# Performance work log

Measured on AMD Instinct MI355X. Metric: run time of the kernel, lower is better.

Reference implementation:

```python
import jax, jax.numpy as jnp
import numpy as np

D_MODEL = 1024
NUM_HEADS = 16
D_HEAD = D_MODEL // NUM_HEADS
LN_EPS = 1e-5


def setup_inputs() -> dict:
    key = jax.random.key(0)
    ks = jax.random.split(key, 10)
    s = 1.0 / np.sqrt(D_MODEL)
    inp = {
        "batch": jax.random.normal(ks[0], (4, 2048, D_MODEL), dtype=jnp.float32),
        "wq": jax.random.uniform(ks[1], (D_MODEL, D_MODEL), jnp.float32, -s, s),
        "bq": jax.random.uniform(ks[2], (D_MODEL,), jnp.float32, -s, s),
        "wk": jax.random.uniform(ks[3], (D_MODEL, D_MODEL), jnp.float32, -s, s),
        "bk": jax.random.uniform(ks[4], (D_MODEL,), jnp.float32, -s, s),
        "wv": jax.random.uniform(ks[5], (D_MODEL, D_MODEL), jnp.float32, -s, s),
        "bv": jax.random.uniform(ks[6], (D_MODEL,), jnp.float32, -s, s),
        "wo": jax.random.uniform(ks[7], (D_MODEL, D_MODEL), jnp.float32, -s, s),
        "bo": jax.random.uniform(ks[8], (D_MODEL,), jnp.float32, -s, s),
        "ln_g": jnp.ones((D_MODEL,), jnp.float32),
        "ln_b": jnp.zeros((D_MODEL,), jnp.float32),
    }
    return inp


def reference(batch, wq, bq, wk, bk, wv, bv, wo, bo, ln_g, ln_b):
    B, S, D = batch.shape
    # QKV projections (torch Linear: x @ W.T + b)
    q = (batch @ wq.T + bq).reshape(B, S, NUM_HEADS, D_HEAD)
    k = (batch @ wk.T + bk).reshape(B, S, NUM_HEADS, D_HEAD)
    v = (batch @ wv.T + bv).reshape(B, S, NUM_HEADS, D_HEAD)
    # attention scores [B, H, S, S]
    scores = jnp.einsum("bqhd,bkhd->bhqk", q, k) / np.sqrt(D_HEAD).astype(np.float32)
    # (original masked_fill is not in-place -> mask has no effect; omitted)
    probs = jax.nn.softmax(scores, axis=-1)
    attn = jnp.einsum("bhqk,bkhd->bqhd", probs, v).reshape(B, S, D)
    residual = attn @ wo.T + bo  # dropout = identity (eval mode)
    x = batch + residual
    mu = jnp.mean(x, axis=-1, keepdims=True)
    var = jnp.mean(jnp.square(x - mu), axis=-1, keepdims=True)
    return (x - mu) / jnp.sqrt(var + LN_EPS) * ln_g + ln_b
```

## Files before the change

kernel.cpp:

```cpp
#include <hip/hip_runtime.h>

typedef __bf16 bf16_t;
typedef __bf16 v8bf __attribute__((ext_vector_type(8)));
typedef __bf16 v4bf __attribute__((ext_vector_type(4)));
typedef float  v4f  __attribute__((ext_vector_type(4)));

#define D_MODEL 1024
#define NHEAD   16
#define DHEAD   64
#define SEQ     2048
#define BATCH   4
#define ROWS    (BATCH*SEQ)

#define GLD16(g, l) __builtin_amdgcn_global_load_lds( \
    (const __attribute__((address_space(1))) void*)(g), \
    (__attribute__((address_space(3))) void*)(l), 16, 0, 0)

#define BAR asm volatile("s_barrier" ::: "memory")

__global__ __launch_bounds__(256) void k_prep(const float* __restrict__ batch,
                                              const float* __restrict__ wq,
                                              const float* __restrict__ wk,
                                              const float* __restrict__ wv,
                                              const float* __restrict__ wo,
                                              const float* __restrict__ bq,
                                              const float* __restrict__ bk,
                                              const float* __restrict__ bv,
                                              bf16_t* __restrict__ Xb,
                                              bf16_t* __restrict__ Wqkv,
                                              bf16_t* __restrict__ Wob,
                                              float* __restrict__ bqkv) {
    int t = threadIdx.x;
    for (int bid = blockIdx.x; bid < 12300; bid += 2048) {
        const float* src; bf16_t* dst; int idx;
        if (bid < 8192)       { src = batch; dst = Xb;             idx = bid * 256 + t; }
        else if (bid < 9216)  { src = wq;    dst = Wqkv;           idx = (bid - 8192) * 256 + t; }
        else if (bid < 10240) { src = wk;    dst = Wqkv + 1048576; idx = (bid - 9216) * 256 + t; }
        else if (bid < 11264) { src = wv;    dst = Wqkv + 2097152; idx = (bid - 10240) * 256 + t; }
        else if (bid < 12288) { src = wo;    dst = Wob;            idx = (bid - 11264) * 256 + t; }
        else {
            int i = (bid - 12288) * 256 + t;
            if (i < 1024) bqkv[i] = bq[i];
            else if (i < 2048) bqkv[i] = bk[i - 1024];
            else if (i < 3072) bqkv[i] = bv[i - 2048];
            continue;
        }
        float4 f = ((const float4*)src)[idx];
        v4bf o;
        o[0] = (bf16_t)f.x; o[1] = (bf16_t)f.y; o[2] = (bf16_t)f.z; o[3] = (bf16_t)f.w;
        ((v4bf*)dst)[idx] = o;
    }
}

__global__ __launch_bounds__(512, 2) void k_gemm256(
    const bf16_t* __restrict__ A, const bf16_t* __restrict__ Bm,
    const float* __restrict__ bias, bf16_t* __restrict__ C, float qmul)
{
    __shared__ bf16_t As[2][2][256 * 32];
    __shared__ bf16_t Bs[2][2][256 * 32];

    const int K = 1024;
    int bid = blockIdx.x;
    int wg = (bid & 7) * 48 + (bid >> 3);
    int m_idx = wg / 12, n_idx = wg % 12;
    int m0 = m_idx << 8, n0 = n_idx << 8;

    int t = threadIdx.x;
    int lane = t & 63, quad = lane >> 4, ln = lane & 15;
    int w = t >> 6, wr = w >> 2, wc = w & 3;

    int cl = (t & 3) ^ ((t >> 3) & 3);
    const bf16_t* Ag = A  + (size_t)(m0 + (t >> 2)) * K + cl * 8;
    const bf16_t* Bg = Bm + (size_t)(n0 + (t >> 2)) * K + cl * 8;
    int wb = w << 9;

#define STA(bufv, khv, kc) { const bf16_t* g_ = Ag + (kc) + ((khv) << 5); \
    GLD16(g_, &As[bufv][khv][wb]); GLD16(g_ + 131072, &As[bufv][khv][wb + 4096]); }
#define STB(bufv, khv, kc) { const bf16_t* g_ = Bg + (kc) + ((khv) << 5); \
    GLD16(g_, &Bs[bufv][khv][wb]); GLD16(g_ + 131072, &Bs[bufv][khv][wb + 4096]); }

    int rsw = (quad ^ ((ln >> 1) & 3)) << 3;
    int aofs = (wr * 128 + ln) * 32 + rsw;
    int bofs = (wc * 64 + ln) * 32 + rsw;

#define LDA(dst, bufv, mhv) { \
    dst[0] = *(const v8bf*)&AB_[aofs + (mhv) * 2048]; \
    dst[1] = *(const v8bf*)&AB_[aofs + (mhv) * 2048 + 512]; \
    dst[2] = *(const v8bf*)&AB_[aofs + (mhv) * 2048 + 1024]; \
    dst[3] = *(const v8bf*)&AB_[aofs + (mhv) * 2048 + 1536]; }
#define LDAF(dst, bufv, khv, mhv) { const bf16_t* AB_ = &As[bufv][khv][0]; LDA(dst, bufv, mhv) }
#define LDBF(dst, bufv, khv) { const bf16_t* BB_ = &Bs[bufv][khv][0]; \
    dst[0] = *(const v8bf*)&BB_[bofs]; \
    dst[1] = *(const v8bf*)&BB_[bofs + 512]; \
    dst[2] = *(const v8bf*)&BB_[bofs + 1024]; \
    dst[3] = *(const v8bf*)&BB_[bofs + 1536]; }

    v4f acc[8][4];
#pragma unroll
    for (int i = 0; i < 8; i++)
#pragma unroll
        for (int j = 0; j < 4; j++) acc[i][j] = (v4f){0.f, 0.f, 0.f, 0.f};

    v8bf aX[4], aY[4], bX[4], bY[4];

#define MF(AC, BC, M0) \
    __builtin_amdgcn_s_setprio(1); \
    acc[(M0)+0][0] = __builtin_amdgcn_mfma_f32_16x16x32_bf16(AC[0], BC[0], acc[(M0)+0][0], 0, 0, 0); \
    acc[(M0)+0][1] = __builtin_amdgcn_mfma_f32_16x16x32_bf16(AC[0], BC[1], acc[(M0)+0][1], 0, 0, 0); \
    acc[(M0)+0][2] = __builtin_amdgcn_mfma_f32_16x16x32_bf16(AC[0], BC[2], acc[(M0)+0][2], 0, 0, 0); \
    acc[(M0)+0][3] = __builtin_amdgcn_mfma_f32_16x16x32_bf16(AC[0], BC[3], acc[(M0)+0][3], 0, 0, 0); \
    acc[(M0)+1][0] = __builtin_amdgcn_mfma_f32_16x16x32_bf16(AC[1], BC[0], acc[(M0)+1][0], 0, 0, 0); \
    acc[(M0)+1][1] = __builtin_amdgcn_mfma_f32_16x16x32_bf16(AC[1], BC[1], acc[(M0)+1][1], 0, 0, 0); \
    acc[(M0)+1][2] = __builtin_amdgcn_mfma_f32_16x16x32_bf16(AC[1], BC[2], acc[(M0)+1][2], 0, 0, 0); \
    acc[(M0)+1][3] = __builtin_amdgcn_mfma_f32_16x16x32_bf16(AC[1], BC[3], acc[(M0)+1][3], 0, 0, 0); \
    acc[(M0)+2][0] = __builtin_amdgcn_mfma_f32_16x16x32_bf16(AC[2], BC[0], acc[(M0)+2][0], 0, 0, 0); \
    acc[(M0)+2][1] = __builtin_amdgcn_mfma_f32_16x16x32_bf16(AC[2], BC[1], acc[(M0)+2][1], 0, 0, 0); \
    acc[(M0)+2][2] = __builtin_amdgcn_mfma_f32_16x16x32_bf16(AC[2], BC[2], acc[(M0)+2][2], 0, 0, 0); \
    acc[(M0)+2][3] = __builtin_amdgcn_mfma_f32_16x16x32_bf16(AC[2], BC[3], acc[(M0)+2][3], 0, 0, 0); \
    acc[(M0)+3][0] = __builtin_amdgcn_mfma_f32_16x16x32_bf16(AC[3], BC[0], acc[(M0)+3][0], 0, 0, 0); \
    acc[(M0)+3][1] = __builtin_amdgcn_mfma_f32_16x16x32_bf16(AC[3], BC[1], acc[(M0)+3][1], 0, 0, 0); \
    acc[(M0)+3][2] = __builtin_amdgcn_mfma_f32_16x16x32_bf16(AC[3], BC[2], acc[(M0)+3][2], 0, 0, 0); \
    acc[(M0)+3][3] = __builtin_amdgcn_mfma_f32_16x16x32_bf16(AC[3], BC[3], acc[(M0)+3][3], 0, 0, 0); \
    __builtin_amdgcn_s_setprio(0);

#define TAIL_W6 { asm volatile("s_waitcnt vmcnt(6)" ::: "memory"); BAR; __builtin_amdgcn_sched_barrier(0); }
#define TAIL_W4 { asm volatile("s_waitcnt vmcnt(4)" ::: "memory"); BAR; __builtin_amdgcn_sched_barrier(0); }
#define TAIL_W0 { asm volatile("s_waitcnt vmcnt(0)" ::: "memory"); BAR; __builtin_amdgcn_sched_barrier(0); }
#define TAIL_B  { BAR; __builtin_amdgcn_sched_barrier(0); }

    STA(0, 0, 0); STB(0, 0, 0);
    STA(0, 1, 0); STB(0, 1, 0);
    STA(1, 0, 64); STB(1, 0, 64);
    asm volatile("s_waitcnt vmcnt(8)" ::: "memory");
    BAR; __builtin_amdgcn_sched_barrier(0);
    LDAF(aX, 0, 0, 0); LDBF(bX, 0, 0);

#define TILE(b, kc, S1, S2, S3, S4, T1, T3, P4B, P4LD) \
    S1; LDAF(aY, b, 0, 1);                    MF(aX, bX, 0); T1; \
    S2; LDBF(bY, b, 1); LDAF(aX, b, 1, 0);    MF(aY, bX, 4); TAIL_B; \
    S3; LDAF(aY, b, 1, 1);                    MF(aX, bY, 0); T3; \
    S4; if (P4LD) { LDBF(bX, P4B, 0); LDAF(aX, P4B, 0, 0); } \
                                              MF(aY, bY, 4); TAIL_B;

    int kb = 0;
#pragma unroll 1
    for (int tp = 0; tp < 7; ++tp, kb += 128) {
        TILE(0, kb, STA(1, 1, kb + 64), STB(1, 1, kb + 64),
                    STA(0, 0, kb + 128), STB(0, 0, kb + 128),
                    TAIL_W6, TAIL_W6, 1, 1)
        TILE(1, kb + 64, STA(0, 1, kb + 128), STB(0, 1, kb + 128),
                         STA(1, 0, kb + 192), STB(1, 0, kb + 192),
                         TAIL_W6, TAIL_W6, 0, 1)
    }
    TILE(0, 896, STA(1, 1, 960), STB(1, 1, 960), , ,
                 TAIL_W6, TAIL_W4, 1, 1)
    { const int b = 1;
      LDAF(aY, b, 0, 1);                    MF(aX, bX, 0); TAIL_W0;
      LDBF(bY, b, 1); LDAF(aX, b, 1, 0);    MF(aY, bX, 4); TAIL_B;
      LDAF(aY, b, 1, 1);                    MF(aX, bY, 0); TAIL_B;
                                            MF(aY, bY, 4);
    }

#undef TILE
#undef MF
#undef TAIL_W6
#undef TAIL_W4
#undef TAIL_W0
#undef TAIL_B
#undef LDA
#undef LDAF
#undef LDBF
#undef STA
#undef STB

#pragma unroll
    for (int m = 0; m < 8; m++) {
#pragma unroll
        for (int r = 0; r < 4; r++) {
            int row = m0 + wr * 128 + m * 16 + quad * 4 + r;
#pragma unroll
            for (int n = 0; n < 4; n++) {
                int col = n0 + wc * 64 + n * 16 + ln;
                float v = acc[m][n][r] + bias[col];
                if (col < 1024) v *= qmul;
                C[(size_t)row * 3072 + col] = (bf16_t)v;
            }
        }
    }
}

__global__ __launch_bounds__(256, 3) void k_gemm_bt(
    const bf16_t* __restrict__ A, const bf16_t* __restrict__ Bm,
    const float* __restrict__ bias, const float* __restrict__ resid,
    bf16_t* __restrict__ Cb, float* __restrict__ Cf,
    int M, int N, int K, int qcols, float qmul)
{
    __shared__ bf16_t As[3][128 * 32];
    __shared__ bf16_t Bs[3][128 * 32];

    int nTile = N >> 7;
    int x = blockIdx.x & 7, g = blockIdx.x >> 3;
    int n_idx = g % nTile;
    int m_idx = (g / nTile) * 8 + x;
    int m0 = m_idx << 7;
    int n0 = n_idx << 7;
    int t = threadIdx.x;
    int w = t >> 6, lane = t & 63, quad = lane >> 4, ln = lane & 15;
    int wm = (w >> 1) << 6, wn = (w & 1) << 6;

    int srow = lane >> 2;
    int scol = ((lane & 3) ^ ((lane >> 3) & 3)) << 3;
    const bf16_t* Ag0 = A  + (size_t)(m0 + w * 16 +      srow) * K + scol;
    const bf16_t* Ag1 = A  + (size_t)(m0 + w * 16 + 64 + srow) * K + scol;
    const bf16_t* Bg0 = Bm + (size_t)(n0 + w * 16 +      srow) * K + scol;
    const bf16_t* Bg1 = Bm + (size_t)(n0 + w * 16 + 64 + srow) * K + scol;
    int lo0 = (w * 16) * 32, lo1 = (w * 16 + 64) * 32;

    v4f acc[4][4];
#pragma unroll
    for (int i = 0; i < 4; i++)
#pragma unroll
        for (int j = 0; j < 4; j++) acc[i][j] = (v4f){0.f, 0.f, 0.f, 0.f};

    bf16_t* aPrev = As[2]; bf16_t* aCur = As[0]; bf16_t* aNext = As[1];
    bf16_t* bPrev = Bs[2]; bf16_t* bCur = Bs[0]; bf16_t* bNext = Bs[1];

    GLD16(Ag0, aCur + lo0);
    GLD16(Ag1, aCur + lo1);
    GLD16(Bg0, bCur + lo0);
    GLD16(Bg1, bCur + lo1);
    GLD16(Ag0 + 32, aNext + lo0);
    GLD16(Ag1 + 32, aNext + lo1);
    GLD16(Bg0 + 32, bNext + lo0);
    GLD16(Bg1 + 32, bNext + lo1);

    int sw = (ln >> 1) & 3;
    for (int k0 = 0; k0 < K; k0 += 32) {
        if (k0 + 32 < K) asm volatile("s_waitcnt vmcnt(4)" ::: "memory");
        else             asm volatile("s_waitcnt vmcnt(0)" ::: "memory");
        __builtin_amdgcn_s_barrier();
        __builtin_amdgcn_sched_barrier(0);
        if (k0 + 64 < K) {
            GLD16(Ag0 + k0 + 64, aPrev + lo0);
            GLD16(Ag1 + k0 + 64, aPrev + lo1);
            GLD16(Bg0 + k0 + 64, bPrev + lo0);
            GLD16(Bg1 + k0 + 64, bPrev + lo1);
        }
        v8bf af[4], bfr[4];
#pragma unroll
        for (int mt = 0; mt < 4; mt++)
            af[mt] = *(const v8bf*)&aCur[(wm + mt * 16 + ln) * 32 + ((quad ^ sw) << 3)];
#pragma unroll
        for (int nt = 0; nt < 4; nt++)
            bfr[nt] = *(const v8bf*)&bCur[(wn + nt * 16 + ln) * 32 + ((quad ^ sw) << 3)];
#pragma unroll
        for (int mt = 0; mt < 4; mt++)
#pragma unroll
            for (int nt = 0; nt < 4; nt++)
                acc[mt][nt] = __builtin_amdgcn_mfma_f32_16x16x32_bf16(af[mt], bfr[nt], acc[mt][nt], 0, 0, 0);
        bf16_t* ta = aPrev; aPrev = aCur; aCur = aNext; aNext = ta;
        bf16_t* tb = bPrev; bPrev = bCur; bCur = bNext; bNext = tb;
    }

#pragma unroll
    for (int mt = 0; mt < 4; mt++) {
#pragma unroll
        for (int r = 0; r < 4; r++) {
            int row = m0 + wm + mt * 16 + quad * 4 + r;
#pragma unroll
            for (int nt = 0; nt < 4; nt++) {
                int col = n0 + wn + nt * 16 + ln;
                float v = acc[mt][nt][r] + bias[col];
                if (Cf) Cf[(size_t)row * N + col] = v + resid[(size_t)row * N + col];
                else {
                    if (col < qcols) v *= qmul;
                    Cb[(size_t)row * N + col] = (bf16_t)v;
                }
            }
        }
    }
}

__global__ __launch_bounds__(256) void k_transpose_v(const bf16_t* __restrict__ qkv,
                                                     bf16_t* __restrict__ vt) {
    __shared__ bf16_t tile[64 * 72];
    int bid = blockIdx.x;
    int st = bid & 31, bh = bid >> 5, b = bh >> 4, h = bh & 15;
    int t = threadIdx.x;
    const bf16_t* src = qkv + (size_t)(b * SEQ + st * 64) * 3072 + 2048 + h * 64;
#pragma unroll
    for (int i = 0; i < 2; i++) {
        int c = t + i * 256, row = c >> 3, c8 = (c & 7) << 3;
        *(uint4*)&tile[row * 72 + c8] = *(const uint4*)(src + (size_t)row * 3072 + c8);
    }
    __syncthreads();
    bf16_t* dst = vt + (size_t)bh * DHEAD * SEQ + st * 64;
#pragma unroll
    for (int i = 0; i < 2; i++) {
        int c = t + i * 256, d = c >> 3, s8 = (c & 7) << 3;
        v8bf o;
#pragma unroll
        for (int j = 0; j < 8; j++) o[j] = tile[(s8 + j) * 72 + d];
        *(v8bf*)(dst + (size_t)d * SEQ + s8) = o;
    }
}

__global__ __launch_bounds__(256, 4) void k_attn(const bf16_t* __restrict__ qkv,
                                                 const bf16_t* __restrict__ vt,
                                                 bf16_t* __restrict__ attn) {
    __shared__ bf16_t Ks[2][64 * 64];
    __shared__ bf16_t Vs[2][64 * 64];

    int bid = blockIdx.x;
    int xcd = bid & 7, g = bid >> 3;
    int qt = g & 15;
    int bh = ((g >> 4) << 3) | xcd;
    int b = bh >> 4, h = bh & 15;
    int t = threadIdx.x, w = t >> 6, lane = t & 63, quad = lane >> 4, ln = lane & 15;
    int q0 = qt * 128 + w * 32;

    v8bf qf[2][2];
#pragma unroll
    for (int qs = 0; qs < 2; qs++) {
        const bf16_t* Qp = qkv + (size_t)(b * SEQ + q0 + qs * 16 + ln) * 3072 + h * 64 + quad * 8;
        qf[qs][0] = *(const v8bf*)Qp;
        qf[qs][1] = *(const v8bf*)(Qp + 32);
    }

    int srow = lane >> 3;
    int scolK = ((lane & 7) ^ ((lane >> 3) & 3) ^ ((w & 1) << 2)) << 3;
    int scolV = ((lane & 7) ^ (lane >> 3)) << 3;
    const bf16_t* Kg0 = qkv + (size_t)(b * SEQ + w * 8 +      srow) * 3072 + 1024 + h * 64 + scolK;
    const bf16_t* Kg1 = qkv + (size_t)(b * SEQ + w * 8 + 32 + srow) * 3072 + 1024 + h * 64 + scolK;
    const bf16_t* Vg0 = vt + (size_t)bh * DHEAD * SEQ + (size_t)(w * 8 +      srow) * SEQ + scolV;
    const bf16_t* Vg1 = vt + (size_t)bh * DHEAD * SEQ + (size_t)(w * 8 + 32 + srow) * SEQ + scolV;
    int ko0 = (w * 8) * 64, ko1 = (w * 8 + 32) * 64;

    int gk = (ln & 3) | (((ln >> 2) & 1) << 2);
    int gv = ln & 7;
    int rrbase = ((ln >> 2) << 3) + (ln & 3);
    int o0 = (rrbase) * 64,       o1 = (rrbase + 4) * 64;
    int o2 = (rrbase + 32) * 64,  o3 = (rrbase + 36) * 64;

    const v4f z4 = (v4f){0.f, 0.f, 0.f, 0.f};
    v8bf ones8;
#pragma unroll
    for (int j = 0; j < 8; j++) ones8[j] = (bf16_t)1.0f;

    v4f o[2][4];
#pragma unroll
    for (int qs = 0; qs < 2; qs++)
#pragma unroll
        for (int d = 0; d < 4; d++) o[qs][d] = z4;
    v4f den[2] = {z4, z4};

    GLD16(Kg0, &Ks[0][ko0]);
    GLD16(Kg1, &Ks[0][ko1]);
    GLD16(Vg0, &Vs[0][ko0]);
    GLD16(Vg1, &Vs[0][ko1]);

    int buf = 0;
    for (int kt = 0; kt < SEQ; kt += 64, buf ^= 1) {
        __syncthreads();
        if (kt + 64 < SEQ) {
            GLD16(Kg0 + (size_t)(kt + 64) * 3072, &Ks[buf ^ 1][ko0]);
            GLD16(Kg1 + (size_t)(kt + 64) * 3072, &Ks[buf ^ 1][ko1]);
            GLD16(Vg0 + kt + 64, &Vs[buf ^ 1][ko0]);
            GLD16(Vg1 + kt + 64, &Vs[buf ^ 1][ko1]);
        }

        const bf16_t* Kb = &Ks[buf][0];
        v4f s0[4], s1[4];
        int rof[4] = {o0, o1, o2, o3};
#pragma unroll
        for (int nt = 0; nt < 4; nt++) {
            v8bf kf0 = *(const v8bf*)&Kb[rof[nt] + ((quad ^ gk) << 3)];
            v8bf kf1 = *(const v8bf*)&Kb[rof[nt] + (((quad | 4) ^ gk) << 3)];
            s0[nt] = __builtin_amdgcn_mfma_f32_16x16x32_bf16(kf0, qf[0][0], z4, 0, 0, 0);
            s0[nt] = __builtin_amdgcn_mfma_f32_16x16x32_bf16(kf1, qf[0][1], s0[nt], 0, 0, 0);
            s1[nt] = __builtin_amdgcn_mfma_f32_16x16x32_bf16(kf0, qf[1][0], z4, 0, 0, 0);
            s1[nt] = __builtin_amdgcn_mfma_f32_16x16x32_bf16(kf1, qf[1][1], s1[nt], 0, 0, 0);
        }

#pragma unroll
        for (int tk = 0; tk < 2; tk++) {
            v8bf vfd[4];
#pragma unroll
            for (int d = 0; d < 4; d++)
                vfd[d] = *(const v8bf*)&Vs[buf][(d * 16 + ln) * 64 + (((tk * 4 + quad) ^ gv) << 3)];
#pragma unroll
            for (int qs = 0; qs < 2; qs++) {
                v4f* s = qs ? s1 : s0;
                float e0 = __builtin_amdgcn_exp2f(s[2 * tk][0]);
                float e1 = __builtin_amdgcn_exp2f(s[2 * tk][1]);
                float e2 = __builtin_amdgcn_exp2f(s[2 * tk][2]);
                float e3 = __builtin_amdgcn_exp2f(s[2 * tk][3]);
                float e4 = __builtin_amdgcn_exp2f(s[2 * tk + 1][0]);
                float e5 = __builtin_amdgcn_exp2f(s[2 * tk + 1][1]);
                float e6 = __builtin_amdgcn_exp2f(s[2 * tk + 1][2]);
                float e7 = __builtin_amdgcn_exp2f(s[2 * tk + 1][3]);
                v8bf pf;
                pf[0] = (bf16_t)e0; pf[1] = (bf16_t)e1; pf[2] = (bf16_t)e2; pf[3] = (bf16_t)e3;
                pf[4] = (bf16_t)e4; pf[5] = (bf16_t)e5; pf[6] = (bf16_t)e6; pf[7] = (bf16_t)e7;
                den[qs] = __builtin_amdgcn_mfma_f32_16x16x32_bf16(pf, ones8, den[qs], 0, 0, 0);
#pragma unroll
                for (int d = 0; d < 4; d++)
                    o[qs][d] = __builtin_amdgcn_mfma_f32_16x16x32_bf16(pf, vfd[d], o[qs][d], 0, 0, 0);
            }
        }
    }

#pragma unroll
    for (int qs = 0; qs < 2; qs++) {
        int rowg = b * SEQ + q0 + qs * 16;
#pragma unroll
        for (int r = 0; r < 4; r++) {
            float inv = 1.f / den[qs][r];
#pragma unroll
            for (int d = 0; d < 4; d++)
                attn[(size_t)(rowg + quad * 4 + r) * D_MODEL + h * 64 + d * 16 + ln] =
                    (bf16_t)(o[qs][d][r] * inv);
        }
    }
}

__global__ __launch_bounds__(256) void k_layernorm(const float* __restrict__ y,
                                                   const float* __restrict__ g,
                                                   const float* __restrict__ beta,
                                                   float* __restrict__ out) {
    __shared__ float rs[4], rq[4];
    int row = blockIdx.x, t = threadIdx.x;
    int w = t >> 6, lane = t & 63;
    float4 v = ((const float4*)(y + (size_t)row * D_MODEL))[t];
    float s = v.x + v.y + v.z + v.w;
    float q = v.x * v.x + v.y * v.y + v.z * v.z + v.w * v.w;
#pragma unroll
    for (int off = 1; off < 64; off <<= 1) {
        s += __shfl_xor(s, off);
        q += __shfl_xor(q, off);
    }
    if (lane == 0) { rs[w] = s; rq[w] = q; }
    __syncthreads();
    s = rs[0] + rs[1] + rs[2] + rs[3];
    q = rq[0] + rq[1] + rq[2] + rq[3];
    float mu = s * (1.f / D_MODEL);
    float var = q * (1.f / D_MODEL) - mu * mu;
    float rstd = rsqrtf(var + 1e-5f);
    float4 gg = ((const float4*)g)[t];
    float4 bb = ((const float4*)beta)[t];
    float4 o;
    o.x = (v.x - mu) * rstd * gg.x + bb.x;
    o.y = (v.y - mu) * rstd * gg.y + bb.y;
    o.z = (v.z - mu) * rstd * gg.z + bb.z;
    o.w = (v.w - mu) * rstd * gg.w + bb.w;
    ((float4*)(out + (size_t)row * D_MODEL))[t] = o;
}

extern "C" void kernel_launch(void* const* d_in, const int* in_sizes, int n_in,
                              void* d_out, int out_size, void* d_ws, size_t ws_size,
                              hipStream_t stream) {
    const float* batch = (const float*)d_in[0];
    const float* wq = (const float*)d_in[1];
    const float* bq = (const float*)d_in[2];
    const float* wk = (const float*)d_in[3];
    const float* bk = (const float*)d_in[4];
    const float* wv = (const float*)d_in[5];
    const float* bv = (const float*)d_in[6];
    const float* wo = (const float*)d_in[7];
    const float* bo = (const float*)d_in[8];
    const float* ln_g = (const float*)d_in[9];
    const float* ln_b = (const float*)d_in[10];
    float* out = (float*)d_out;

    char* ws = (char*)d_ws;
    size_t offXb   = 0;
    size_t offWqkv = offXb + (size_t)ROWS * D_MODEL * 2;
    size_t offWo   = offWqkv + (size_t)3072 * 1024 * 2;
    size_t offBias = offWo + (size_t)1024 * 1024 * 2;
    size_t offQKV  = offBias + 3072 * 4;
    size_t offAttn = offQKV + (size_t)ROWS * 3072 * 2;
    size_t total   = offAttn + (size_t)ROWS * D_MODEL * 2;
    if (ws_size < total) return;

    bf16_t* Xb   = (bf16_t*)(ws + offXb);
    bf16_t* Vt   = (bf16_t*)(ws + offXb);
    bf16_t* Wqkv = (bf16_t*)(ws + offWqkv);
    bf16_t* Wob  = (bf16_t*)(ws + offWo);
    float*  bqkv = (float*)(ws + offBias);
    bf16_t* qkv  = (bf16_t*)(ws + offQKV);
    float*  y    = (float*)(ws + offQKV);
    bf16_t* attn = (bf16_t*)(ws + offAttn);

    const float SC = 0.125f * 1.44269504088896f;

    k_prep<<<2048, 256, 0, stream>>>(batch, wq, wk, wv, wo, bq, bk, bv,
                                     Xb, Wqkv, Wob, bqkv);
    k_gemm256<<<384, 512, 0, stream>>>(Xb, Wqkv, bqkv, qkv, SC);
    k_transpose_v<<<2048, 256, 0, stream>>>(qkv, Vt);
    k_attn<<<1024, 256, 0, stream>>>(qkv, Vt, attn);
    k_gemm_bt<<<64 * 8, 256, 0, stream>>>(attn, Wob, bo, batch, nullptr, y,
                                          8192, 1024, 1024, 0, 1.0f);
    k_layernorm<<<8192, 256, 0, stream>>>(y, ln_g, ln_b, out);
}
```

Baseline: 296.7 us.

## Use two-stage LDS double buffering in GEMM and relax attention occupancy bound

The GEMM's three-buffer LDS ring becomes a simpler two-buffer ping-pong. The hand-placed s_waitcnt and raw barriers are replaced by a __syncthreads at the top of each K step, which then prefetches only the next tile. This cuts the GEMM's LDS footprint and control logic, but it shrinks the prefetch distance, so more global-load latency may be exposed. Separately, the attention kernel's launch-bounds minimum waves is lowered from 4 to 2, giving the compiler more registers per thread at the cost of occupancy.

```diff
diff --git a/kernel.cpp b/kernel.cpp
--- a/kernel.cpp
+++ b/kernel.cpp
@@ -195,8 +195,8 @@
     bf16_t* __restrict__ Cb, float* __restrict__ Cf,
     int M, int N, int K, int qcols, float qmul)
 {
-    __shared__ bf16_t As[3][128 * 32];
-    __shared__ bf16_t Bs[3][128 * 32];
+    __shared__ bf16_t As[2][128 * 32];
+    __shared__ bf16_t Bs[2][128 * 32];
 
     int nTile = N >> 7;
     int x = blockIdx.x & 7, g = blockIdx.x >> 3;
@@ -222,44 +222,33 @@
 #pragma unroll
         for (int j = 0; j < 4; j++) acc[i][j] = (v4f){0.f, 0.f, 0.f, 0.f};
 
-    bf16_t* aPrev = As[2]; bf16_t* aCur = As[0]; bf16_t* aNext = As[1];
-    bf16_t* bPrev = Bs[2]; bf16_t* bCur = Bs[0]; bf16_t* bNext = Bs[1];
-
-    GLD16(Ag0, aCur + lo0);
-    GLD16(Ag1, aCur + lo1);
-    GLD16(Bg0, bCur + lo0);
-    GLD16(Bg1, bCur + lo1);
-    GLD16(Ag0 + 32, aNext + lo0);
-    GLD16(Ag1 + 32, aNext + lo1);
-    GLD16(Bg0 + 32, bNext + lo0);
-    GLD16(Bg1 + 32, bNext + lo1);
+    GLD16(Ag0, &As[0][lo0]);
+    GLD16(Ag1, &As[0][lo1]);
+    GLD16(Bg0, &Bs[0][lo0]);
+    GLD16(Bg1, &Bs[0][lo1]);
 
     int sw = (ln >> 1) & 3;
-    for (int k0 = 0; k0 < K; k0 += 32) {
-        if (k0 + 32 < K) asm volatile("s_waitcnt vmcnt(4)" ::: "memory");
-        else             asm volatile("s_waitcnt vmcnt(0)" ::: "memory");
-        __builtin_amdgcn_s_barrier();
-        __builtin_amdgcn_sched_barrier(0);
-        if (k0 + 64 < K) {
-            GLD16(Ag0 + k0 + 64, aPrev + lo0);
-            GLD16(Ag1 + k0 + 64, aPrev + lo1);
-            GLD16(Bg0 + k0 + 64, bPrev + lo0);
-            GLD16(Bg1 + k0 + 64, bPrev + lo1);
+    int buf = 0;
+    for (int k0 = 0; k0 < K; k0 += 32, buf ^= 1) {
+        __syncthreads();
+        if (k0 + 32 < K) {
+            GLD16(Ag0 + k0 + 32, &As[buf ^ 1][lo0]);
+            GLD16(Ag1 + k0 + 32, &As[buf ^ 1][lo1]);
+            GLD16(Bg0 + k0 + 32, &Bs[buf ^ 1][lo0]);
+            GLD16(Bg1 + k0 + 32, &Bs[buf ^ 1][lo1]);
         }
         v8bf af[4], bfr[4];
 #pragma unroll
         for (int mt = 0; mt < 4; mt++)
-            af[mt] = *(const v8bf*)&aCur[(wm + mt * 16 + ln) * 32 + ((quad ^ sw) << 3)];
+            af[mt] = *(const v8bf*)&As[buf][(wm + mt * 16 + ln) * 32 + ((quad ^ sw) << 3)];
 #pragma unroll
         for (int nt = 0; nt < 4; nt++)
-            bfr[nt] = *(const v8bf*)&bCur[(wn + nt * 16 + ln) * 32 + ((quad ^ sw) << 3)];
+            bfr[nt] = *(const v8bf*)&Bs[buf][(wn + nt * 16 + ln) * 32 + ((quad ^ sw) << 3)];
 #pragma unroll
         for (int mt = 0; mt < 4; mt++)
 #pragma unroll
             for (int nt = 0; nt < 4; nt++)
                 acc[mt][nt] = __builtin_amdgcn_mfma_f32_16x16x32_bf16(af[mt], bfr[nt], acc[mt][nt], 0, 0, 0);
-        bf16_t* ta = aPrev; aPrev = aCur; aCur = aNext; aNext = ta;
-        bf16_t* tb = bPrev; bPrev = bCur; bCur = bNext; bNext = tb;
     }
 
 #pragma unroll
@@ -305,7 +294,7 @@
     }
 }
 
-__global__ __launch_bounds__(256, 4) void k_attn(const bf16_t* __restrict__ qkv,
+__global__ __launch_bounds__(256, 2) void k_attn(const bf16_t* __restrict__ qkv,
                                                  const bf16_t* __restrict__ vt,
                                                  bf16_t* __restrict__ attn) {
     __shared__ bf16_t Ks[2][64 * 64];
```

Result: no change. 300.1 us (+1.1%).
